# Optimization experiments

Hardware: AMD Instinct MI355X
Metric: run time of the kernel (lower is better)

The kernel has to match this reference:

```python
import jax, jax.numpy as jnp
import numpy as np

EMBED_DIM = 1024
NUM_HEADS = 16
HEAD_DIM = EMBED_DIM // NUM_HEADS
SCALE = HEAD_DIM ** -0.5


def setup_inputs() -> dict:
    key = jax.random.key(0)
    k_x, k_qkv, k_proj = jax.random.split(key, 3)
    x = jax.random.normal(k_x, (2, 2048, EMBED_DIM), dtype=jnp.float32)
    # nn.Linear weights: [out_features, in_features]
    w_qkv = jax.random.normal(k_qkv, (3 * EMBED_DIM, EMBED_DIM), dtype=jnp.float32) * (EMBED_DIM ** -0.5)
    w_proj = jax.random.normal(k_proj, (EMBED_DIM, EMBED_DIM), dtype=jnp.float32) * (EMBED_DIM ** -0.5)
    return {"x": x, "w_qkv": w_qkv, "w_proj": w_proj}


def reference(x, w_qkv, w_proj):
    B, N, C = x.shape
    # fused QKV projection: [B,N,3C]
    qkv = jnp.einsum('bnc,oc->bno', x, w_qkv)
    qkv = qkv.reshape(B, N, 3, NUM_HEADS, HEAD_DIM)
    q, k, v = jnp.moveaxis(qkv, 2, 0)  # each [B, N, H, D]
    q = q.transpose(0, 2, 1, 3)  # [B, H, N, D]
    k = k.transpose(0, 2, 1, 3)
    v = v.transpose(0, 2, 1, 3)
    # scaled dot-product attention (eval mode: dropout_p=0, non-causal)
    scores = jnp.einsum('bhqd,bhkd->bhqk', q, k) * SCALE
    attn = jax.nn.softmax(scores, axis=-1)
    out = jnp.einsum('bhqk,bhkd->bhqd', attn, v)  # [B, H, N, D]
    out = out.transpose(0, 2, 1, 3).reshape(B, N, C)
    return jnp.einsum('bnc,oc->bno', out, w_proj)
```

## Files before the change

kernel.cpp:

```cpp
#include <hip/hip_runtime.h>
#include <hip/hip_bf16.h>

typedef __bf16 bf16;
typedef __bf16 bf16x8 __attribute__((ext_vector_type(8)));
typedef __bf16 bf16x4 __attribute__((ext_vector_type(4)));
typedef float f32x4 __attribute__((ext_vector_type(4)));

#define MFMA16(a, b, c) __builtin_amdgcn_mfma_f32_16x16x32_bf16(a, b, c, 0, 0, 0)

__device__ __forceinline__ void gll(const bf16* g, bf16* l) {
    __builtin_amdgcn_global_load_lds(
        (const __attribute__((address_space(1))) unsigned int*)g,
        (__attribute__((address_space(3))) unsigned int*)l, 16, 0, 0);
}

__global__ void cvt_all(const float* __restrict__ x, const float* __restrict__ wq,
                        const float* __restrict__ wp, bf16* __restrict__ xb,
                        bf16* __restrict__ wqb, bf16* __restrict__ wpb) {
    int i = blockIdx.x * 256 + threadIdx.x;
    const float4* s; bf16* d; int j;
    if (i < 1048576)                { s = (const float4*)x;  d = xb;  j = i; }
    else if (i < 1048576 + 786432)  { s = (const float4*)wq; d = wqb; j = i - 1048576; }
    else                            { s = (const float4*)wp; d = wpb; j = i - 1835008; }
    float4 f = s[j];
    bf16x4 o; o[0] = (bf16)f.x; o[1] = (bf16)f.y; o[2] = (bf16)f.z; o[3] = (bf16)f.w;
    ((bf16x4*)d)[j] = o;
}

#define QSCALE 0.18033688f

__global__ __launch_bounds__(256, 3) void gemm_qkv(
    const bf16* __restrict__ A, const bf16* __restrict__ Bm,
    bf16* __restrict__ qo, bf16* __restrict__ ko, bf16* __restrict__ vo)
{
    __shared__ bf16 As[2][128 * 32];
    __shared__ bf16 Bs[2][128 * 32];
    const int tid = threadIdx.x;
    const int wave = tid >> 6, lane = tid & 63;
    const int lrow = lane & 15, quad = lane >> 4;
    const int wm = (wave >> 1) * 64, wn = (wave & 1) * 64;
    const int srow = tid >> 2;
    const int scol = ((tid & 3) ^ (srow & 3)) * 8;
    const int fsw = (quad ^ (lrow & 3)) * 8;

    const bf16* Ap = A + (long)(blockIdx.x * 128 + srow) * 1024 + scol;
    const bf16* Bp = Bm + (long)(blockIdx.y * 128 + srow) * 1024 + scol;

    f32x4 acc[4][4] = {};
    const int gm0 = blockIdx.x * 128 + wm;
    const int go0 = blockIdx.y * 128 + wn;

    gll(Ap, &As[0][tid * 8]);  gll(Ap + 64 * 1024, &As[0][2048 + tid * 8]);
    gll(Bp, &Bs[0][tid * 8]);  gll(Bp + 64 * 1024, &Bs[0][2048 + tid * 8]);

    if (blockIdx.y < 16) {
        for (int i = 0; i < 32; i++) {
            const int cur = i & 1;
            __syncthreads();
            if (i < 31) {
                const int k0 = (i + 1) * 32;
                gll(Ap + k0, &As[cur ^ 1][tid * 8]);
                gll(Ap + 64 * 1024 + k0, &As[cur ^ 1][2048 + tid * 8]);
                gll(Bp + k0, &Bs[cur ^ 1][tid * 8]);
                gll(Bp + 64 * 1024 + k0, &Bs[cur ^ 1][2048 + tid * 8]);
            }
            bf16x8 af[4], bfr[4];
#pragma unroll
            for (int ii = 0; ii < 4; ii++) af[ii] = *(const bf16x8*)&As[cur][(wm + ii * 16 + lrow) * 32 + fsw];
#pragma unroll
            for (int j = 0; j < 4; j++) bfr[j] = *(const bf16x8*)&Bs[cur][(wn + j * 16 + lrow) * 32 + fsw];
#pragma unroll
            for (int ii = 0; ii < 4; ii++)
#pragma unroll
                for (int j = 0; j < 4; j++)
                    acc[ii][j] = MFMA16(bfr[j], af[ii], acc[ii][j]);
        }
        const bool isQ = blockIdx.y < 8;
        bf16* dst = isQ ? qo : ko;
        const float sc = isQ ? QSCALE : 1.0f;
#pragma unroll
        for (int i = 0; i < 4; i++) {
            int gm = gm0 + i * 16 + lrow;
            int b = gm >> 11, n = gm & 2047;
#pragma unroll
            for (int j = 0; j < 4; j++) {
                int ob = go0 + j * 16 + quad * 4;
                int rem = ob & 1023;
                int h = rem >> 6, d0 = rem & 63;
                bf16x4 pk;
#pragma unroll
                for (int r = 0; r < 4; r++) pk[r] = (bf16)(acc[i][j][r] * sc);
                *(bf16x4*)&dst[((long)(b * 16 + h) * 2048 + n) * 64 + d0] = pk;
            }
        }
    } else {
        for (int i = 0; i < 32; i++) {
            const int cur = i & 1;
            __syncthreads();
            if (i < 31) {
                const int k0 = (i + 1) * 32;
                gll(Ap + k0, &As[cur ^ 1][tid * 8]);
                gll(Ap + 64 * 1024 + k0, &As[cur ^ 1][2048 + tid * 8]);
                gll(Bp + k0, &Bs[cur ^ 1][tid * 8]);
                gll(Bp + 64 * 1024 + k0, &Bs[cur ^ 1][2048 + tid * 8]);
            }
            bf16x8 af[4], bfr[4];
#pragma unroll
            for (int ii = 0; ii < 4; ii++) af[ii] = *(const bf16x8*)&As[cur][(wm + ii * 16 + lrow) * 32 + fsw];
#pragma unroll
            for (int j = 0; j < 4; j++) bfr[j] = *(const bf16x8*)&Bs[cur][(wn + j * 16 + lrow) * 32 + fsw];
#pragma unroll
            for (int ii = 0; ii < 4; ii++)
#pragma unroll
                for (int j = 0; j < 4; j++)
                    acc[ii][j] = MFMA16(af[ii], bfr[j], acc[ii][j]);
        }
#pragma unroll
        for (int i = 0; i < 4; i++) {
            int gmb = gm0 + i * 16 + quad * 4;
            int b = gmb >> 11, nb = gmb & 2047;
#pragma unroll
            for (int j = 0; j < 4; j++) {
                int o = go0 + j * 16 + lrow;
                int rem = o & 1023;
                int h = rem >> 6, d = rem & 63;
                bf16x4 pk;
#pragma unroll
                for (int r = 0; r < 4; r++) pk[r] = (bf16)acc[i][j][r];
                *(bf16x4*)&vo[(((long)(b * 16 + h)) * 64 + d) * 2048 + nb] = pk;
            }
        }
    }
}

__global__ __launch_bounds__(256, 2) void attn_kernel(
    const bf16* __restrict__ q, const bf16* __restrict__ k,
    const bf16* __restrict__ vt, bf16* __restrict__ o)
{
    __shared__ bf16 Ks[2][64 * 64];
    __shared__ bf16 Vs[2][64 * 64];
    __shared__ bf16 Ps[4][32 * 72];

    const int tid = threadIdx.x, wave = tid >> 6, lane = tid & 63;
    const int lrow = lane & 15, quad = lane >> 4;
    const int bh = blockIdx.x & 31, qt = blockIdx.x >> 5;
    const bf16* Qp = q + ((long)bh * 2048 + qt * 128 + wave * 32) * 64;
    const bf16* Kp = k + (long)bh * 2048 * 64;
    const bf16* Vp = vt + (long)bh * 64 * 2048;

    const int sr = tid >> 3;
    const int scc = ((tid & 7) ^ (sr & 7)) * 8;
    const int ksw = (lrow & 7);

    bf16x8 qf[2][2];
#pragma unroll
    for (int t = 0; t < 2; t++)
#pragma unroll
        for (int ks = 0; ks < 2; ks++)
            qf[t][ks] = *(const bf16x8*)&Qp[(t * 16 + lrow) * 64 + ks * 32 + quad * 8];

#pragma unroll
    for (int p = 0; p < 2; p++) {
        gll(Kp + (sr + 32 * p) * 64 + scc,          &Ks[0][p * 2048 + tid * 8]);
        gll(Vp + (long)(sr + 32 * p) * 2048 + scc,  &Vs[0][p * 2048 + tid * 8]);
    }

    float lsum[2] = {0.0f, 0.0f};
    f32x4 oacc[2][4] = {};
    bf16* Pw = &Ps[wave][0];

    for (int kv = 0; kv < 32; kv++) {
        const int cur = kv & 1;
        __syncthreads();
        if (kv < 31) {
            const bf16* Kn = Kp + (kv + 1) * 4096;
            const bf16* Vn = Vp + (kv + 1) * 64;
#pragma unroll
            for (int p = 0; p < 2; p++) {
                gll(Kn + (sr + 32 * p) * 64 + scc,         &Ks[cur ^ 1][p * 2048 + tid * 8]);
                gll(Vn + (long)(sr + 32 * p) * 2048 + scc, &Vs[cur ^ 1][p * 2048 + tid * 8]);
            }
        }

        f32x4 sacc[2][4] = {};
#pragma unroll
        for (int ks = 0; ks < 2; ks++) {
            bf16x8 kf[4];
#pragma unroll
            for (int n = 0; n < 4; n++)
                kf[n] = *(const bf16x8*)&Ks[cur][(n * 16 + lrow) * 64 + (((ks * 4 + quad) ^ ksw) * 8)];
#pragma unroll
            for (int t = 0; t < 2; t++)
#pragma unroll
                for (int n = 0; n < 4; n++)
                    sacc[t][n] = MFMA16(kf[n], qf[t][ks], sacc[t][n]);
        }

#pragma unroll
        for (int t = 0; t < 2; t++) {
#pragma unroll
            for (int n = 0; n < 4; n++) {
                bf16x4 pk;
#pragma unroll
                for (int r = 0; r < 4; r++) {
                    float p = __builtin_exp2f(sacc[t][n][r]);
                    lsum[t] += p;
                    pk[r] = (bf16)p;
                }
                *(bf16x4*)&Pw[(t * 16 + lrow) * 72 + n * 16 + quad * 4] = pk;
            }
        }

#pragma unroll
        for (int c = 0; c < 2; c++) {
            bf16x8 vf[4];
#pragma unroll
            for (int jd = 0; jd < 4; jd++)
                vf[jd] = *(const bf16x8*)&Vs[cur][(jd * 16 + lrow) * 64 + (((c * 4 + quad) ^ ksw) * 8)];
#pragma unroll
            for (int t = 0; t < 2; t++) {
                bf16x8 pf = *(const bf16x8*)&Pw[(t * 16 + lrow) * 72 + c * 32 + quad * 8];
#pragma unroll
                for (int jd = 0; jd < 4; jd++)
                    oacc[t][jd] = MFMA16(pf, vf[jd], oacc[t][jd]);
            }
        }
    }

#pragma unroll
    for (int t = 0; t < 2; t++) {
        lsum[t] += __shfl_xor(lsum[t], 16, 64);
        lsum[t] += __shfl_xor(lsum[t], 32, 64);
    }

    const int b = bh >> 4, h = bh & 15;
#pragma unroll
    for (int t = 0; t < 2; t++) {
        float linv = 1.0f / lsum[t];
#pragma unroll
        for (int r = 0; r < 4; r++) {
            float lr = __shfl(linv, quad * 4 + r, 64);
#pragma unroll
            for (int jd = 0; jd < 4; jd++)
                Pw[(t * 16 + quad * 4 + r) * 72 + jd * 16 + lrow] = (bf16)(oacc[t][jd][r] * lr);
        }
    }
    const int rr = lane >> 3, cc = (lane & 7) * 8;
#pragma unroll
    for (int p = 0; p < 4; p++) {
        bf16x8 val = *(const bf16x8*)&Pw[(rr + p * 8) * 72 + cc];
        int n = qt * 128 + wave * 32 + rr + p * 8;
        *(bf16x8*)&o[((long)(b * 2048 + n)) * 1024 + h * 64 + cc] = val;
    }
}

__global__ __launch_bounds__(256, 2) void gemm_proj(
    const bf16* __restrict__ A, const bf16* __restrict__ Bm, float* __restrict__ out)
{
    __shared__ bf16 As[2][128 * 32];
    __shared__ bf16 Bs[2][64 * 32];
    const int tid = threadIdx.x;
    const int wave = tid >> 6, lane = tid & 63;
    const int lrow = lane & 15, quad = lane >> 4;
    const int wm = (wave >> 1) * 64, wn = (wave & 1) * 32;
    const int srow = tid >> 2;
    const int scol = ((tid & 3) ^ (srow & 3)) * 8;
    const int fsw = (quad ^ (lrow & 3)) * 8;

    const bf16* Ap = A + (long)(blockIdx.x * 128 + srow) * 1024 + scol;
    const bf16* Bp = Bm + (long)(blockIdx.y * 64 + srow) * 1024 + scol;

    f32x4 acc[4][2] = {};

    gll(Ap, &As[0][tid * 8]);  gll(Ap + 64 * 1024, &As[0][2048 + tid * 8]);
    gll(Bp, &Bs[0][tid * 8]);

    for (int i = 0; i < 32; i++) {
        const int cur = i & 1;
        __syncthreads();
        if (i < 31) {
            const int k0 = (i + 1) * 32;
            gll(Ap + k0, &As[cur ^ 1][tid * 8]);
            gll(Ap + 64 * 1024 + k0, &As[cur ^ 1][2048 + tid * 8]);
            gll(Bp + k0, &Bs[cur ^ 1][tid * 8]);
        }
        bf16x8 af[4], bfr[2];
#pragma unroll
        for (int ii = 0; ii < 4; ii++) af[ii] = *(const bf16x8*)&As[cur][(wm + ii * 16 + lrow) * 32 + fsw];
#pragma unroll
        for (int j = 0; j < 2; j++) bfr[j] = *(const bf16x8*)&Bs[cur][(wn + j * 16 + lrow) * 32 + fsw];
#pragma unroll
        for (int ii = 0; ii < 4; ii++)
#pragma unroll
            for (int j = 0; j < 2; j++)
                acc[ii][j] = MFMA16(bfr[j], af[ii], acc[ii][j]);
    }

    const int gm0 = blockIdx.x * 128 + wm;
    const int go0 = blockIdx.y * 64 + wn;
#pragma unroll
    for (int i = 0; i < 4; i++) {
        int gm = gm0 + i * 16 + lrow;
#pragma unroll
        for (int j = 0; j < 2; j++) {
            int ob = go0 + j * 16 + quad * 4;
            *(f32x4*)&out[(long)gm * 1024 + ob] = acc[i][j];
        }
    }
}

extern "C" void kernel_launch(void* const* d_in, const int* in_sizes, int n_in,
                              void* d_out, int out_size, void* d_ws, size_t ws_size,
                              hipStream_t stream) {
    const float* x      = (const float*)d_in[0];
    const float* w_qkv  = (const float*)d_in[1];
    const float* w_proj = (const float*)d_in[2];
    float* out = (float*)d_out;

    bf16* ws = (bf16*)d_ws;
    bf16* xb     = ws;
    bf16* wqkvb  = xb + 4096 * 1024;
    bf16* wprojb = wqkvb + 3072 * 1024;
    bf16* qb     = wprojb + 1024 * 1024;
    bf16* kb     = qb + 2 * 16 * 2048 * 64;
    bf16* vb     = kb + 2 * 16 * 2048 * 64;
    bf16* ob     = vb + 2 * 16 * 2048 * 64;

    cvt_all<<<8192, 256, 0, stream>>>(x, w_qkv, w_proj, xb, wqkvb, wprojb);
    gemm_qkv<<<dim3(32, 24), 256, 0, stream>>>(xb, wqkvb, qb, kb, vb);
    attn_kernel<<<512, 256, 0, stream>>>(qb, kb, vb, ob);
    gemm_proj<<<dim3(32, 16), 256, 0, stream>>>(ob, wprojb, out);
}
```

Measured before the change: 193.5 us.

## Remap GEMM blocks per XCD and load V fragments directly from global

Both GEMMs now launch a 1D grid and remap the block index so that blocks landing on the same XCD share the same weight column tiles (by), aiming for better L2 reuse across the chiplets. In the attention kernel, V tiles are no longer staged through double-buffered LDS. Each wave instead loads its V fragments straight from global memory into registers at the start of every KV step. This cuts LDS footprint and async copies, but it adds strided global loads with no prefetch that may sit on the critical path.

Measured after the change: 213.3 us. 1.1x slower.

```diff
diff --git a/kernel.cpp b/kernel.cpp
--- a/kernel.cpp
+++ b/kernel.cpp
@@ -43,17 +43,22 @@
     const int scol = ((tid & 3) ^ (srow & 3)) * 8;
     const int fsw = (quad ^ (lrow & 3)) * 8;
 
-    const bf16* Ap = A + (long)(blockIdx.x * 128 + srow) * 1024 + scol;
-    const bf16* Bp = Bm + (long)(blockIdx.y * 128 + srow) * 1024 + scol;
+    const int bidx = blockIdx.x;
+    const int xcd = bidx & 7, slot = bidx >> 3;
+    const int by = xcd * 3 + (slot >> 5);
+    const int bx = slot & 31;
+
+    const bf16* Ap = A + (long)(bx * 128 + srow) * 1024 + scol;
+    const bf16* Bp = Bm + (long)(by * 128 + srow) * 1024 + scol;
 
     f32x4 acc[4][4] = {};
-    const int gm0 = blockIdx.x * 128 + wm;
-    const int go0 = blockIdx.y * 128 + wn;
+    const int gm0 = bx * 128 + wm;
+    const int go0 = by * 128 + wn;
 
     gll(Ap, &As[0][tid * 8]);  gll(Ap + 64 * 1024, &As[0][2048 + tid * 8]);
     gll(Bp, &Bs[0][tid * 8]);  gll(Bp + 64 * 1024, &Bs[0][2048 + tid * 8]);
 
-    if (blockIdx.y < 16) {
+    if (by < 16) {
         for (int i = 0; i < 32; i++) {
             const int cur = i & 1;
             __syncthreads();
@@ -75,7 +80,7 @@
                 for (int j = 0; j < 4; j++)
                     acc[ii][j] = MFMA16(bfr[j], af[ii], acc[ii][j]);
         }
-        const bool isQ = blockIdx.y < 8;
+        const bool isQ = by < 8;
         bf16* dst = isQ ? qo : ko;
         const float sc = isQ ? QSCALE : 1.0f;
 #pragma unroll
@@ -138,7 +143,6 @@
     const bf16* __restrict__ vt, bf16* __restrict__ o)
 {
     __shared__ bf16 Ks[2][64 * 64];
-    __shared__ bf16 Vs[2][64 * 64];
     __shared__ bf16 Ps[4][32 * 72];
 
     const int tid = threadIdx.x, wave = tid >> 6, lane = tid & 63;
@@ -160,10 +164,8 @@
             qf[t][ks] = *(const bf16x8*)&Qp[(t * 16 + lrow) * 64 + ks * 32 + quad * 8];
 
 #pragma unroll
-    for (int p = 0; p < 2; p++) {
-        gll(Kp + (sr + 32 * p) * 64 + scc,          &Ks[0][p * 2048 + tid * 8]);
-        gll(Vp + (long)(sr + 32 * p) * 2048 + scc,  &Vs[0][p * 2048 + tid * 8]);
-    }
+    for (int p = 0; p < 2; p++)
+        gll(Kp + (sr + 32 * p) * 64 + scc, &Ks[0][p * 2048 + tid * 8]);
 
     float lsum[2] = {0.0f, 0.0f};
     f32x4 oacc[2][4] = {};
@@ -174,13 +176,17 @@
         __syncthreads();
         if (kv < 31) {
             const bf16* Kn = Kp + (kv + 1) * 4096;
-            const bf16* Vn = Vp + (kv + 1) * 64;
-#pragma unroll
-            for (int p = 0; p < 2; p++) {
-                gll(Kn + (sr + 32 * p) * 64 + scc,         &Ks[cur ^ 1][p * 2048 + tid * 8]);
-                gll(Vn + (long)(sr + 32 * p) * 2048 + scc, &Vs[cur ^ 1][p * 2048 + tid * 8]);
-            }
-        }
+#pragma unroll
+            for (int p = 0; p < 2; p++)
+                gll(Kn + (sr + 32 * p) * 64 + scc, &Ks[cur ^ 1][p * 2048 + tid * 8]);
+        }
+
+        bf16x8 vf[2][4];
+#pragma unroll
+        for (int c = 0; c < 2; c++)
+#pragma unroll
+            for (int jd = 0; jd < 4; jd++)
+                vf[c][jd] = *(const bf16x8*)&Vp[(long)(jd * 16 + lrow) * 2048 + kv * 64 + c * 32 + quad * 8];
 
         f32x4 sacc[2][4] = {};
 #pragma unroll
@@ -212,19 +218,14 @@
         }
 
 #pragma unroll
-        for (int c = 0; c < 2; c++) {
-            bf16x8 vf[4];
-#pragma unroll
-            for (int jd = 0; jd < 4; jd++)
-                vf[jd] = *(const bf16x8*)&Vs[cur][(jd * 16 + lrow) * 64 + (((c * 4 + quad) ^ ksw) * 8)];
+        for (int c = 0; c < 2; c++)
 #pragma unroll
             for (int t = 0; t < 2; t++) {
                 bf16x8 pf = *(const bf16x8*)&Pw[(t * 16 + lrow) * 72 + c * 32 + quad * 8];
 #pragma unroll
                 for (int jd = 0; jd < 4; jd++)
-                    oacc[t][jd] = MFMA16(pf, vf[jd], oacc[t][jd]);
-            }
-        }
+                    oacc[t][jd] = MFMA16(pf, vf[c][jd], oacc[t][jd]);
+            }
     }
 
 #pragma unroll
@@ -267,8 +268,13 @@
     const int scol = ((tid & 3) ^ (srow & 3)) * 8;
     const int fsw = (quad ^ (lrow & 3)) * 8;
 
-    const bf16* Ap = A + (long)(blockIdx.x * 128 + srow) * 1024 + scol;
-    const bf16* Bp = Bm + (long)(blockIdx.y * 64 + srow) * 1024 + scol;
+    const int bidx = blockIdx.x;
+    const int xcd = bidx & 7, slot = bidx >> 3;
+    const int by = xcd * 2 + (slot >> 5);
+    const int bx = slot & 31;
+
+    const bf16* Ap = A + (long)(bx * 128 + srow) * 1024 + scol;
+    const bf16* Bp = Bm + (long)(by * 64 + srow) * 1024 + scol;
 
     f32x4 acc[4][2] = {};
 
@@ -296,8 +302,8 @@
                 acc[ii][j] = MFMA16(bfr[j], af[ii], acc[ii][j]);
     }
 
-    const int gm0 = blockIdx.x * 128 + wm;
-    const int go0 = blockIdx.y * 64 + wn;
+    const int gm0 = bx * 128 + wm;
+    const int go0 = by * 64 + wn;
 #pragma unroll
     for (int i = 0; i < 4; i++) {
         int gm = gm0 + i * 16 + lrow;
@@ -327,7 +333,7 @@
     bf16* ob     = vb + 2 * 16 * 2048 * 64;
 
     cvt_all<<<8192, 256, 0, stream>>>(x, w_qkv, w_proj, xb, wqkvb, wprojb);
-    gemm_qkv<<<dim3(32, 24), 256, 0, stream>>>(xb, wqkvb, qb, kb, vb);
+    gemm_qkv<<<768, 256, 0, stream>>>(xb, wqkvb, qb, kb, vb);
     attn_kernel<<<512, 256, 0, stream>>>(qb, kb, vb, ob);
-    gemm_proj<<<dim3(32, 16), 256, 0, stream>>>(ob, wprojb, out);
-}
+    gemm_proj<<<512, 256, 0, stream>>>(ob, wprojb, out);
+}
```

## Enlarge GEMM tiles and remap blocks across XCDs for L2 reuse

Applied to the files above, without the earlier changes.

The QKV GEMM moves from 128x128 to 256x128 tiles with 8x4 accumulators per wave, launched on a 1-D grid of 384 blocks. Each XCD handles a contiguous group of output-column tiles so blocks on the same die share weight rows in L2. The projection GEMM moves from 128x64 to 128x128 tiles with a similar XCD-aware 1-D mapping over 256 blocks. This raises arithmetic intensity per LDS load and improves L2 locality. In exchange it adds register pressure (occupancy hint drops to 2 for qkv) and launches fewer blocks, which may leave CUs underfilled.

Measured after the change: 209.7 us. 8.4% more time.

```diff
diff --git a/kernel.cpp b/kernel.cpp
--- a/kernel.cpp
+++ b/kernel.cpp
@@ -29,9 +29,240 @@
 
 #define QSCALE 0.18033688f
 
-__global__ __launch_bounds__(256, 3) void gemm_qkv(
+__global__ __launch_bounds__(256, 2) void gemm_qkv(
     const bf16* __restrict__ A, const bf16* __restrict__ Bm,
     bf16* __restrict__ qo, bf16* __restrict__ ko, bf16* __restrict__ vo)
+{
+    __shared__ bf16 As[2][256 * 32];
+    __shared__ bf16 Bs[2][128 * 32];
+    const int tid = threadIdx.x;
+    const int wave = tid >> 6, lane = tid & 63;
+    const int lrow = lane & 15, quad = lane >> 4;
+    const int wm = (wave >> 1) * 128, wn = (wave & 1) * 64;
+    const int srow = tid >> 2;
+    const int scol = ((tid & 3) ^ (srow & 3)) * 8;
+    const int fsw = (quad ^ (lrow & 3)) * 8;
+
+    const int bidx = blockIdx.x;
+    const int xcd = bidx & 7, slot = bidx >> 3;
+    const int by = xcd * 3 + (slot >> 4);
+    const int bx = slot & 15;
+
+    const bf16* Ap = A + (long)(bx * 256 + srow) * 1024 + scol;
+    const bf16* Bp = Bm + (long)(by * 128 + srow) * 1024 + scol;
+
+    f32x4 acc[8][4] = {};
+    const int gm0 = bx * 256 + wm;
+    const int go0 = by * 128 + wn;
+
+#pragma unroll
+    for (int p = 0; p < 4; p++) gll(Ap + p * 64 * 1024, &As[0][p * 2048 + tid * 8]);
+#pragma unroll
+    for (int p = 0; p < 2; p++) gll(Bp + p * 64 * 1024, &Bs[0][p * 2048 + tid * 8]);
+
+    if (by < 16) {
+        for (int i = 0; i < 32; i++) {
+            const int cur = i & 1;
+            __syncthreads();
+            if (i < 31) {
+                const int k0 = (i + 1) * 32;
+#pragma unroll
+                for (int p = 0; p < 4; p++) gll(Ap + p * 64 * 1024 + k0, &As[cur ^ 1][p * 2048 + tid * 8]);
+#pragma unroll
+                for (int p = 0; p < 2; p++) gll(Bp + p * 64 * 1024 + k0, &Bs[cur ^ 1][p * 2048 + tid * 8]);
+            }
+            bf16x8 bfr[4];
+#pragma unroll
+            for (int j = 0; j < 4; j++) bfr[j] = *(const bf16x8*)&Bs[cur][(wn + j * 16 + lrow) * 32 + fsw];
+#pragma unroll
+            for (int ii = 0; ii < 8; ii++) {
+                bf16x8 af = *(const bf16x8*)&As[cur][(wm + ii * 16 + lrow) * 32 + fsw];
+#pragma unroll
+                for (int j = 0; j < 4; j++)
+                    acc[ii][j] = MFMA16(bfr[j], af, acc[ii][j]);
+            }
+        }
+        const bool isQ = by < 8;
+        bf16* dst = isQ ? qo : ko;
+        const float sc = isQ ? QSCALE : 1.0f;
+#pragma unroll
+        for (int i = 0; i < 8; i++) {
+            int gm = gm0 + i * 16 + lrow;
+            int b = gm >> 11, n = gm & 2047;
+#pragma unroll
+            for (int j = 0; j < 4; j++) {
+                int ob = go0 + j * 16 + quad * 4;
+                int rem = ob & 1023;
+                int h = rem >> 6, d0 = rem & 63;
+                bf16x4 pk;
+#pragma unroll
+                for (int r = 0; r < 4; r++) pk[r] = (bf16)(acc[i][j][r] * sc);
+                *(bf16x4*)&dst[((long)(b * 16 + h) * 2048 + n) * 64 + d0] = pk;
+            }
+        }
+    } else {
+        for (int i = 0; i < 32; i++) {
+            const int cur = i & 1;
+            __syncthreads();
+            if (i < 31) {
+                const int k0 = (i + 1) * 32;
+#pragma unroll
+                for (int p = 0; p < 4; p++) gll(Ap + p * 64 * 1024 + k0, &As[cur ^ 1][p * 2048 + tid * 8]);
+#pragma unroll
+                for (int p = 0; p < 2; p++) gll(Bp + p * 64 * 1024 + k0, &Bs[cur ^ 1][p * 2048 + tid * 8]);
+            }
+            bf16x8 bfr[4];
+#pragma unroll
+            for (int j = 0; j < 4; j++) bfr[j] = *(const bf16x8*)&Bs[cur][(wn + j * 16 + lrow) * 32 + fsw];
+#pragma unroll
+            for (int ii = 0; ii < 8; ii++) {
+                bf16x8 af = *(const bf16x8*)&As[cur][(wm + ii * 16 + lrow) * 32 + fsw];
+#pragma unroll
+                for (int j = 0; j < 4; j++)
+                    acc[ii][j] = MFMA16(af, bfr[j], acc[ii][j]);
+            }
+        }
+#pragma unroll
+        for (int i = 0; i < 8; i++) {
+            int gmb = gm0 + i * 16 + quad * 4;
+            int b = gmb >> 11, nb = gmb & 2047;
+#pragma unroll
+            for (int j = 0; j < 4; j++) {
+                int o = go0 + j * 16 + lrow;
+                int rem = o & 1023;
+                int h = rem >> 6, d = rem & 63;
+                bf16x4 pk;
+#pragma unroll
+                for (int r = 0; r < 4; r++) pk[r] = (bf16)acc[i][j][r];
+                *(bf16x4*)&vo[(((long)(b * 16 + h)) * 64 + d) * 2048 + nb] = pk;
+            }
+        }
+    }
+}
+
+__global__ __launch_bounds__(256, 2) void attn_kernel(
+    const bf16* __restrict__ q, const bf16* __restrict__ k,
+    const bf16* __restrict__ vt, bf16* __restrict__ o)
+{
+    __shared__ bf16 Ks[2][64 * 64];
+    __shared__ bf16 Vs[2][64 * 64];
+    __shared__ bf16 Ps[4][32 * 72];
+
+    const int tid = threadIdx.x, wave = tid >> 6, lane = tid & 63;
+    const int lrow = lane & 15, quad = lane >> 4;
+    const int bh = blockIdx.x & 31, qt = blockIdx.x >> 5;
+    const bf16* Qp = q + ((long)bh * 2048 + qt * 128 + wave * 32) * 64;
+    const bf16* Kp = k + (long)bh * 2048 * 64;
+    const bf16* Vp = vt + (long)bh * 64 * 2048;
+
+    const int sr = tid >> 3;
+    const int scc = ((tid & 7) ^ (sr & 7)) * 8;
+    const int ksw = (lrow & 7);
+
+    bf16x8 qf[2][2];
+#pragma unroll
+    for (int t = 0; t < 2; t++)
+#pragma unroll
+        for (int ks = 0; ks < 2; ks++)
+            qf[t][ks] = *(const bf16x8*)&Qp[(t * 16 + lrow) * 64 + ks * 32 + quad * 8];
+
+#pragma unroll
+    for (int p = 0; p < 2; p++) {
+        gll(Kp + (sr + 32 * p) * 64 + scc,          &Ks[0][p * 2048 + tid * 8]);
+        gll(Vp + (long)(sr + 32 * p) * 2048 + scc,  &Vs[0][p * 2048 + tid * 8]);
+    }
+
+    float lsum[2] = {0.0f, 0.0f};
+    f32x4 oacc[2][4] = {};
+    bf16* Pw = &Ps[wave][0];
+
+    for (int kv = 0; kv < 32; kv++) {
+        const int cur = kv & 1;
+        __syncthreads();
+        if (kv < 31) {
+            const bf16* Kn = Kp + (kv + 1) * 4096;
+            const bf16* Vn = Vp + (kv + 1) * 64;
+#pragma unroll
+            for (int p = 0; p < 2; p++) {
+                gll(Kn + (sr + 32 * p) * 64 + scc,         &Ks[cur ^ 1][p * 2048 + tid * 8]);
+                gll(Vn + (long)(sr + 32 * p) * 2048 + scc, &Vs[cur ^ 1][p * 2048 + tid * 8]);
+            }
+        }
+
+        f32x4 sacc[2][4] = {};
+#pragma unroll
+        for (int ks = 0; ks < 2; ks++) {
+            bf16x8 kf[4];
+#pragma unroll
+            for (int n = 0; n < 4; n++)
+                kf[n] = *(const bf16x8*)&Ks[cur][(n * 16 + lrow) * 64 + (((ks * 4 + quad) ^ ksw) * 8)];
+#pragma unroll
+            for (int t = 0; t < 2; t++)
+#pragma unroll
+                for (int n = 0; n < 4; n++)
+                    sacc[t][n] = MFMA16(kf[n], qf[t][ks], sacc[t][n]);
+        }
+
+#pragma unroll
+        for (int t = 0; t < 2; t++) {
+#pragma unroll
+            for (int n = 0; n < 4; n++) {
+                bf16x4 pk;
+#pragma unroll
+                for (int r = 0; r < 4; r++) {
+                    float p = __builtin_exp2f(sacc[t][n][r]);
+                    lsum[t] += p;
+                    pk[r] = (bf16)p;
+                }
+                *(bf16x4*)&Pw[(t * 16 + lrow) * 72 + n * 16 + quad * 4] = pk;
+            }
+        }
+
+#pragma unroll
+        for (int c = 0; c < 2; c++) {
+            bf16x8 vf[4];
+#pragma unroll
+            for (int jd = 0; jd < 4; jd++)
+                vf[jd] = *(const bf16x8*)&Vs[cur][(jd * 16 + lrow) * 64 + (((c * 4 + quad) ^ ksw) * 8)];
+#pragma unroll
+            for (int t = 0; t < 2; t++) {
+                bf16x8 pf = *(const bf16x8*)&Pw[(t * 16 + lrow) * 72 + c * 32 + quad * 8];
+#pragma unroll
+                for (int jd = 0; jd < 4; jd++)
+                    oacc[t][jd] = MFMA16(pf, vf[jd], oacc[t][jd]);
+            }
+        }
+    }
+
+#pragma unroll
+    for (int t = 0; t < 2; t++) {
+        lsum[t] += __shfl_xor(lsum[t], 16, 64);
+        lsum[t] += __shfl_xor(lsum[t], 32, 64);
+    }
+
+    const int b = bh >> 4, h = bh & 15;
+#pragma unroll
+    for (int t = 0; t < 2; t++) {
+        float linv = 1.0f / lsum[t];
+#pragma unroll
+        for (int r = 0; r < 4; r++) {
+            float lr = __shfl(linv, quad * 4 + r, 64);
+#pragma unroll
+            for (int jd = 0; jd < 4; jd++)
+                Pw[(t * 16 + quad * 4 + r) * 72 + jd * 16 + lrow] = (bf16)(oacc[t][jd][r] * lr);
+        }
+    }
+    const int rr = lane >> 3, cc = (lane & 7) * 8;
+#pragma unroll
+    for (int p = 0; p < 4; p++) {
+        bf16x8 val = *(const bf16x8*)&Pw[(rr + p * 8) * 72 + cc];
+        int n = qt * 128 + wave * 32 + rr + p * 8;
+        *(bf16x8*)&o[((long)(b * 2048 + n)) * 1024 + h * 64 + cc] = val;
+    }
+}
+
+__global__ __launch_bounds__(256, 3) void gemm_proj(
+    const bf16* __restrict__ A, const bf16* __restrict__ Bm, float* __restrict__ out)
 {
     __shared__ bf16 As[2][128 * 32];
     __shared__ bf16 Bs[2][128 * 32];
@@ -43,237 +274,18 @@
     const int scol = ((tid & 3) ^ (srow & 3)) * 8;
     const int fsw = (quad ^ (lrow & 3)) * 8;
 
-    const bf16* Ap = A + (long)(blockIdx.x * 128 + srow) * 1024 + scol;
-    const bf16* Bp = Bm + (long)(blockIdx.y * 128 + srow) * 1024 + scol;
+    const int bidx = blockIdx.x;
+    const int xcd = bidx & 7, slot = bidx >> 3;
+    const int by = xcd;
+    const int bx = slot;
+
+    const bf16* Ap = A + (long)(bx * 128 + srow) * 1024 + scol;
+    const bf16* Bp = Bm + (long)(by * 128 + srow) * 1024 + scol;
 
     f32x4 acc[4][4] = {};
-    const int gm0 = blockIdx.x * 128 + wm;
-    const int go0 = blockIdx.y * 128 + wn;
 
     gll(Ap, &As[0][tid * 8]);  gll(Ap + 64 * 1024, &As[0][2048 + tid * 8]);
     gll(Bp, &Bs[0][tid * 8]);  gll(Bp + 64 * 1024, &Bs[0][2048 + tid * 8]);
-
-    if (blockIdx.y < 16) {
-        for (int i = 0; i < 32; i++) {
-            const int cur = i & 1;
-            __syncthreads();
-            if (i < 31) {
-                const int k0 = (i + 1) * 32;
-                gll(Ap + k0, &As[cur ^ 1][tid * 8]);
-                gll(Ap + 64 * 1024 + k0, &As[cur ^ 1][2048 + tid * 8]);
-                gll(Bp + k0, &Bs[cur ^ 1][tid * 8]);
-                gll(Bp + 64 * 1024 + k0, &Bs[cur ^ 1][2048 + tid * 8]);
-            }
-            bf16x8 af[4], bfr[4];
-#pragma unroll
-            for (int ii = 0; ii < 4; ii++) af[ii] = *(const bf16x8*)&As[cur][(wm + ii * 16 + lrow) * 32 + fsw];
-#pragma unroll
-            for (int j = 0; j < 4; j++) bfr[j] = *(const bf16x8*)&Bs[cur][(wn + j * 16 + lrow) * 32 + fsw];
-#pragma unroll
-            for (int ii = 0; ii < 4; ii++)
-#pragma unroll
-                for (int j = 0; j < 4; j++)
-                    acc[ii][j] = MFMA16(bfr[j], af[ii], acc[ii][j]);
-        }
-        const bool isQ = blockIdx.y < 8;
-        bf16* dst = isQ ? qo : ko;
-        const float sc = isQ ? QSCALE : 1.0f;
-#pragma unroll
-        for (int i = 0; i < 4; i++) {
-            int gm = gm0 + i * 16 + lrow;
-            int b = gm >> 11, n = gm & 2047;
-#pragma unroll
-            for (int j = 0; j < 4; j++) {
-                int ob = go0 + j * 16 + quad * 4;
-                int rem = ob & 1023;
-                int h = rem >> 6, d0 = rem & 63;
-                bf16x4 pk;
-#pragma unroll
-                for (int r = 0; r < 4; r++) pk[r] = (bf16)(acc[i][j][r] * sc);
-                *(bf16x4*)&dst[((long)(b * 16 + h) * 2048 + n) * 64 + d0] = pk;
-            }
-        }
-    } else {
-        for (int i = 0; i < 32; i++) {
-            const int cur = i & 1;
-            __syncthreads();
-            if (i < 31) {
-                const int k0 = (i + 1) * 32;
-                gll(Ap + k0, &As[cur ^ 1][tid * 8]);
-                gll(Ap + 64 * 1024 + k0, &As[cur ^ 1][2048 + tid * 8]);
-                gll(Bp + k0, &Bs[cur ^ 1][tid * 8]);
-                gll(Bp + 64 * 1024 + k0, &Bs[cur ^ 1][2048 + tid * 8]);
-            }
-            bf16x8 af[4], bfr[4];
-#pragma unroll
-            for (int ii = 0; ii < 4; ii++) af[ii] = *(const bf16x8*)&As[cur][(wm + ii * 16 + lrow) * 32 + fsw];
-#pragma unroll
-            for (int j = 0; j < 4; j++) bfr[j] = *(const bf16x8*)&Bs[cur][(wn + j * 16 + lrow) * 32 + fsw];
-#pragma unroll
-            for (int ii = 0; ii < 4; ii++)
-#pragma unroll
-                for (int j = 0; j < 4; j++)
-                    acc[ii][j] = MFMA16(af[ii], bfr[j], acc[ii][j]);
-        }
-#pragma unroll
-        for (int i = 0; i < 4; i++) {
-            int gmb = gm0 + i * 16 + quad * 4;
-            int b = gmb >> 11, nb = gmb & 2047;
-#pragma unroll
-            for (int j = 0; j < 4; j++) {
-                int o = go0 + j * 16 + lrow;
-                int rem = o & 1023;
-                int h = rem >> 6, d = rem & 63;
-                bf16x4 pk;
-#pragma unroll
-                for (int r = 0; r < 4; r++) pk[r] = (bf16)acc[i][j][r];
-                *(bf16x4*)&vo[(((long)(b * 16 + h)) * 64 + d) * 2048 + nb] = pk;
-            }
-        }
-    }
-}
-
-__global__ __launch_bounds__(256, 2) void attn_kernel(
-    const bf16* __restrict__ q, const bf16* __restrict__ k,
-    const bf16* __restrict__ vt, bf16* __restrict__ o)
-{
-    __shared__ bf16 Ks[2][64 * 64];
-    __shared__ bf16 Vs[2][64 * 64];
-    __shared__ bf16 Ps[4][32 * 72];
-
-    const int tid = threadIdx.x, wave = tid >> 6, lane = tid & 63;
-    const int lrow = lane & 15, quad = lane >> 4;
-    const int bh = blockIdx.x & 31, qt = blockIdx.x >> 5;
-    const bf16* Qp = q + ((long)bh * 2048 + qt * 128 + wave * 32) * 64;
-    const bf16* Kp = k + (long)bh * 2048 * 64;
-    const bf16* Vp = vt + (long)bh * 64 * 2048;
-
-    const int sr = tid >> 3;
-    const int scc = ((tid & 7) ^ (sr & 7)) * 8;
-    const int ksw = (lrow & 7);
-
-    bf16x8 qf[2][2];
-#pragma unroll
-    for (int t = 0; t < 2; t++)
-#pragma unroll
-        for (int ks = 0; ks < 2; ks++)
-            qf[t][ks] = *(const bf16x8*)&Qp[(t * 16 + lrow) * 64 + ks * 32 + quad * 8];
-
-#pragma unroll
-    for (int p = 0; p < 2; p++) {
-        gll(Kp + (sr + 32 * p) * 64 + scc,          &Ks[0][p * 2048 + tid * 8]);
-        gll(Vp + (long)(sr + 32 * p) * 2048 + scc,  &Vs[0][p * 2048 + tid * 8]);
-    }
-
-    float lsum[2] = {0.0f, 0.0f};
-    f32x4 oacc[2][4] = {};
-    bf16* Pw = &Ps[wave][0];
-
-    for (int kv = 0; kv < 32; kv++) {
-        const int cur = kv & 1;
-        __syncthreads();
-        if (kv < 31) {
-            const bf16* Kn = Kp + (kv + 1) * 4096;
-            const bf16* Vn = Vp + (kv + 1) * 64;
-#pragma unroll
-            for (int p = 0; p < 2; p++) {
-                gll(Kn + (sr + 32 * p) * 64 + scc,         &Ks[cur ^ 1][p * 2048 + tid * 8]);
-                gll(Vn + (long)(sr + 32 * p) * 2048 + scc, &Vs[cur ^ 1][p * 2048 + tid * 8]);
-            }
-        }
-
-        f32x4 sacc[2][4] = {};
-#pragma unroll
-        for (int ks = 0; ks < 2; ks++) {
-            bf16x8 kf[4];
-#pragma unroll
-            for (int n = 0; n < 4; n++)
-                kf[n] = *(const bf16x8*)&Ks[cur][(n * 16 + lrow) * 64 + (((ks * 4 + quad) ^ ksw) * 8)];
-#pragma unroll
-            for (int t = 0; t < 2; t++)
-#pragma unroll
-                for (int n = 0; n < 4; n++)
-                    sacc[t][n] = MFMA16(kf[n], qf[t][ks], sacc[t][n]);
-        }
-
-#pragma unroll
-        for (int t = 0; t < 2; t++) {
-#pragma unroll
-            for (int n = 0; n < 4; n++) {
-                bf16x4 pk;
-#pragma unroll
-                for (int r = 0; r < 4; r++) {
-                    float p = __builtin_exp2f(sacc[t][n][r]);
-                    lsum[t] += p;
-                    pk[r] = (bf16)p;
-                }
-                *(bf16x4*)&Pw[(t * 16 + lrow) * 72 + n * 16 + quad * 4] = pk;
-            }
-        }
-
-#pragma unroll
-        for (int c = 0; c < 2; c++) {
-            bf16x8 vf[4];
-#pragma unroll
-            for (int jd = 0; jd < 4; jd++)
-                vf[jd] = *(const bf16x8*)&Vs[cur][(jd * 16 + lrow) * 64 + (((c * 4 + quad) ^ ksw) * 8)];
-#pragma unroll
-            for (int t = 0; t < 2; t++) {
-                bf16x8 pf = *(const bf16x8*)&Pw[(t * 16 + lrow) * 72 + c * 32 + quad * 8];
-#pragma unroll
-                for (int jd = 0; jd < 4; jd++)
-                    oacc[t][jd] = MFMA16(pf, vf[jd], oacc[t][jd]);
-            }
-        }
-    }
-
-#pragma unroll
-    for (int t = 0; t < 2; t++) {
-        lsum[t] += __shfl_xor(lsum[t], 16, 64);
-        lsum[t] += __shfl_xor(lsum[t], 32, 64);
-    }
-
-    const int b = bh >> 4, h = bh & 15;
-#pragma unroll
-    for (int t = 0; t < 2; t++) {
-        float linv = 1.0f / lsum[t];
-#pragma unroll
-        for (int r = 0; r < 4; r++) {
-            float lr = __shfl(linv, quad * 4 + r, 64);
-#pragma unroll
-            for (int jd = 0; jd < 4; jd++)
-                Pw[(t * 16 + quad * 4 + r) * 72 + jd * 16 + lrow] = (bf16)(oacc[t][jd][r] * lr);
-        }
-    }
-    const int rr = lane >> 3, cc = (lane & 7) * 8;
-#pragma unroll
-    for (int p = 0; p < 4; p++) {
-        bf16x8 val = *(const bf16x8*)&Pw[(rr + p * 8) * 72 + cc];
-        int n = qt * 128 + wave * 32 + rr + p * 8;
-        *(bf16x8*)&o[((long)(b * 2048 + n)) * 1024 + h * 64 + cc] = val;
-    }
-}
-
-__global__ __launch_bounds__(256, 2) void gemm_proj(
-    const bf16* __restrict__ A, const bf16* __restrict__ Bm, float* __restrict__ out)
-{
-    __shared__ bf16 As[2][128 * 32];
-    __shared__ bf16 Bs[2][64 * 32];
-    const int tid = threadIdx.x;
-    const int wave = tid >> 6, lane = tid & 63;
-    const int lrow = lane & 15, quad = lane >> 4;
-    const int wm = (wave >> 1) * 64, wn = (wave & 1) * 32;
-    const int srow = tid >> 2;
-    const int scol = ((tid & 3) ^ (srow & 3)) * 8;
-    const int fsw = (quad ^ (lrow & 3)) * 8;
-
-    const bf16* Ap = A + (long)(blockIdx.x * 128 + srow) * 1024 + scol;
-    const bf16* Bp = Bm + (long)(blockIdx.y * 64 + srow) * 1024 + scol;
-
-    f32x4 acc[4][2] = {};
-
-    gll(Ap, &As[0][tid * 8]);  gll(Ap + 64 * 1024, &As[0][2048 + tid * 8]);
-    gll(Bp, &Bs[0][tid * 8]);
 
     for (int i = 0; i < 32; i++) {
         const int cur = i & 1;
@@ -283,26 +295,27 @@
             gll(Ap + k0, &As[cur ^ 1][tid * 8]);
             gll(Ap + 64 * 1024 + k0, &As[cur ^ 1][2048 + tid * 8]);
             gll(Bp + k0, &Bs[cur ^ 1][tid * 8]);
-        }
-        bf16x8 af[4], bfr[2];
+            gll(Bp + 64 * 1024 + k0, &Bs[cur ^ 1][2048 + tid * 8]);
+        }
+        bf16x8 af[4], bfr[4];
 #pragma unroll
         for (int ii = 0; ii < 4; ii++) af[ii] = *(const bf16x8*)&As[cur][(wm + ii * 16 + lrow) * 32 + fsw];
 #pragma unroll
-        for (int j = 0; j < 2; j++) bfr[j] = *(const bf16x8*)&Bs[cur][(wn + j * 16 + lrow) * 32 + fsw];
+        for (int j = 0; j < 4; j++) bfr[j] = *(const bf16x8*)&Bs[cur][(wn + j * 16 + lrow) * 32 + fsw];
 #pragma unroll
         for (int ii = 0; ii < 4; ii++)
 #pragma unroll
-            for (int j = 0; j < 2; j++)
+            for (int j = 0; j < 4; j++)
                 acc[ii][j] = MFMA16(bfr[j], af[ii], acc[ii][j]);
     }
 
-    const int gm0 = blockIdx.x * 128 + wm;
-    const int go0 = blockIdx.y * 64 + wn;
+    const int gm0 = bx * 128 + wm;
+    const int go0 = by * 128 + wn;
 #pragma unroll
     for (int i = 0; i < 4; i++) {
         int gm = gm0 + i * 16 + lrow;
 #pragma unroll
-        for (int j = 0; j < 2; j++) {
+        for (int j = 0; j < 4; j++) {
             int ob = go0 + j * 16 + quad * 4;
             *(f32x4*)&out[(long)gm * 1024 + ob] = acc[i][j];
         }
@@ -327,7 +340,7 @@
     bf16* ob     = vb + 2 * 16 * 2048 * 64;
 
     cvt_all<<<8192, 256, 0, stream>>>(x, w_qkv, w_proj, xb, wqkvb, wprojb);
-    gemm_qkv<<<dim3(32, 24), 256, 0, stream>>>(xb, wqkvb, qb, kb, vb);
+    gemm_qkv<<<384, 256, 0, stream>>>(xb, wqkvb, qb, kb, vb);
     attn_kernel<<<512, 256, 0, stream>>>(qb, kb, vb, ob);
-    gemm_proj<<<dim3(32, 16), 256, 0, stream>>>(ob, wprojb, out);
-}
+    gemm_proj<<<256, 256, 0, stream>>>(ob, wprojb, out);
+}
```
